# Performance work log

Hardware: AMD Instinct MI355X
Metric: run time of the kernel (lower is better)

The kernel has to match this reference:

```python
import jax, jax.numpy as jnp
import numpy as np

B, T, D = 4, 2048, 1024
H = 16
HD = D // H  # 64


def setup_inputs() -> dict:
    key = jax.random.key(0)
    ks = jax.random.split(key, 7)
    scale = 1.0 / np.sqrt(D)
    x = jax.random.normal(ks[0], (B, T, D), dtype=jnp.float32)
    # per-head projection weights, stacked over heads: [H, D, HD]
    Wq = jax.random.normal(ks[1], (H, D, HD), dtype=jnp.float32) * scale
    Wk = jax.random.normal(ks[2], (H, D, HD), dtype=jnp.float32) * scale
    Wv = jax.random.normal(ks[3], (H, D, HD), dtype=jnp.float32) * scale
    s_raw = jnp.zeros((H,), dtype=jnp.float32)  # learnable ssmax scale per head
    proj_W = jax.random.normal(ks[4], (D, D), dtype=jnp.float32) * scale
    proj_b = jax.random.normal(ks[5], (D,), dtype=jnp.float32) * 0.01
    return {"x": x, "Wq": Wq, "Wk": Wk, "Wv": Wv, "s_raw": s_raw,
            "proj_W": proj_W, "proj_b": proj_b}


def reference(x, Wq, Wk, Wv, s_raw, proj_W, proj_b):
    # per-head q/k/v: [B, H, T, HD]
    q = jnp.einsum('btd,hde->bhte', x, Wq)
    k = jnp.einsum('btd,hde->bhte', x, Wk)
    v = jnp.einsum('btd,hde->bhte', x, Wv)

    # ssmax: q scaled by softplus(s) * log(position index, 1-based)
    logn = jnp.log(jnp.arange(1, T + 1, dtype=x.dtype))  # [T]
    s = jax.nn.softplus(s_raw)  # [H]
    q = q * (s[None, :, None, None] * logn[None, None, :, None])

    scores = jnp.einsum('bhte,bhse->bhts', q, k) * (HD ** -0.5)
    causal = jnp.tril(jnp.ones((T, T), dtype=bool))
    scores = jnp.where(causal[None, None], scores, -jnp.inf)
    w = jax.nn.softmax(scores, axis=-1)

    out = jnp.einsum('bhts,bhse->bhte', w, v)          # [B, H, T, HD]
    out = out.transpose(0, 2, 1, 3).reshape(B, T, D)    # concat heads
    return out @ proj_W.T + proj_b
```

## Files before the change

kernel.cpp:

```cpp
#include <hip/hip_runtime.h>
#include <hip/hip_bf16.h>

#define Bv 4
#define Tv 2048
#define Dv 1024
#define Hv 16
#define HDv 64
#define Mv (Bv*Tv)

typedef __hip_bfloat16 bf16;
typedef short s8v __attribute__((ext_vector_type(8)));
typedef float f4v __attribute__((ext_vector_type(4)));
typedef float f16a __attribute__((ext_vector_type(16)));

__device__ __forceinline__ unsigned short f2us(float x){
    bf16 h = __float2bfloat16(x);
    return *reinterpret_cast<unsigned short*>(&h);
}
__device__ __forceinline__ unsigned int pack2(float a, float b){
    return (unsigned int)f2us(a) | ((unsigned int)f2us(b) << 16);
}
__device__ __forceinline__ void glds16(const unsigned short* g, unsigned short* lds_base){
    __builtin_amdgcn_global_load_lds(
        (const __attribute__((address_space(1))) unsigned int*)g,
        (__attribute__((address_space(3))) unsigned int*)lds_base, 16, 0, 0);
}

__global__ void cvt_kernel(const float* __restrict__ src,
                           unsigned short* __restrict__ dst, int n4) {
    int i = blockIdx.x * 256 + threadIdx.x;
    if (i < n4) {
        float4 f = *(const float4*)(src + (size_t)i * 4);
        ushort4 o;
        o.x = f2us(f.x); o.y = f2us(f.y); o.z = f2us(f.z); o.w = f2us(f.w);
        *(ushort4*)(dst + (size_t)i * 4) = o;
    }
}

__global__ __launch_bounds__(256) void wt_kernel(
    const float* __restrict__ Wq, const float* __restrict__ Wk,
    const float* __restrict__ Wv, unsigned short* __restrict__ Wt)
{
    const int dt  = blockIdx.x;
    const int h   = blockIdx.y;
    const int sel = blockIdx.z;
    const float* W = (sel == 0) ? Wq : ((sel == 1) ? Wk : Wv);
    const float* Wh = W + (size_t)h * Dv * HDv;
    __shared__ float Tf[64][65];
    const int tid = threadIdx.x;
    for (int l = 0; l < 16; ++l) {
        int idx = tid + l * 256;
        int r = idx >> 6, e = idx & 63;
        Tf[r][e] = Wh[(size_t)(dt * 64 + r) * HDv + e];
    }
    __syncthreads();
    unsigned short* out = Wt + ((size_t)sel * Hv + h) * HDv * Dv;
    for (int l = 0; l < 16; ++l) {
        int idx = tid + l * 256;
        int e = idx >> 6, d = idx & 63;
        out[(size_t)e * Dv + dt * 64 + d] = f2us(Tf[d][e]);
    }
}

__global__ __launch_bounds__(512, 2) void qkv_8ph(
    const unsigned short* __restrict__ xb, const unsigned short* __restrict__ Wc,
    const float* __restrict__ s_raw,
    unsigned short* __restrict__ q, unsigned short* __restrict__ k,
    unsigned short* __restrict__ vT)
{
    extern __shared__ unsigned short smem[];
    const int lid  = blockIdx.x;
    const int xcd  = lid & 7;
    const int slot = lid >> 3;
    const int bm   = xcd * 4 + (slot & 3);
    const int bn   = slot >> 2;
    const int tid = threadIdx.x;
    const int w = tid >> 6, lane = tid & 63;
    const int wm = w >> 2, wn = w & 3;
    const int n16 = lane & 15, quad = lane >> 4, l7 = lane & 7;

    const int row0 = bm * 256, col0 = bn * 256;

    const int sr = lane >> 3;
    const int sc = ((lane & 7) ^ (sr & 7)) * 8;

    f4v acc[8][4];
    f4v zero = {0.f, 0.f, 0.f, 0.f};
    #pragma unroll
    for (int i = 0; i < 8; ++i)
        #pragma unroll
        for (int j = 0; j < 4; ++j) acc[i][j] = zero;

    s8v Ar[8][2];
    s8v Br[4][2];

    auto stageA = [&](int b, int h, int tk){
        const unsigned short* g = xb + ((size_t)(row0 + h*128 + w*16 + sr)) * Dv + tk*64 + sc;
        unsigned short* l = smem + b*32768 + h*8192 + w*1024;
        glds16(g, l);
        glds16(g + 8*Dv, l + 512);
    };
    auto stageB = [&](int b, int h, int tk){
        const unsigned short* g = Wc + ((size_t)(col0 + h*128 + w*16 + sr)) * Dv + tk*64 + sc;
        unsigned short* l = smem + b*32768 + 16384 + h*8192 + w*1024;
        glds16(g, l);
        glds16(g + 8*Dv, l + 512);
    };
    auto readA = [&](int b, int mh){
        #pragma unroll
        for (int mi = 0; mi < 4; ++mi)
            #pragma unroll
            for (int kk = 0; kk < 2; ++kk)
                Ar[mh*4+mi][kk] = *(const s8v*)(smem + b*32768 + wm*8192
                    + ((mh*4+mi)*16 + n16) * 64 + (((kk*4 + quad) ^ l7) * 8));
    };
    auto readB = [&](int b, int nh){
        #pragma unroll
        for (int ni = 0; ni < 2; ++ni)
            #pragma unroll
            for (int kk = 0; kk < 2; ++kk)
                Br[nh*2+ni][kk] = *(const s8v*)(smem + b*32768 + 16384 + (wn>>1)*8192
                    + ((wn&1)*64 + (nh*2+ni)*16 + n16) * 64 + (((kk*4 + quad) ^ l7) * 8));
    };
    auto quadMM = [&](int mh, int nh){
        #pragma unroll
        for (int kk = 0; kk < 2; ++kk)
            #pragma unroll
            for (int mi = 0; mi < 4; ++mi)
                #pragma unroll
                for (int ni = 0; ni < 2; ++ni)
                    acc[mh*4+mi][nh*2+ni] = __builtin_amdgcn_mfma_f32_16x16x32_bf16(
                        Ar[mh*4+mi][kk], Br[nh*2+ni][kk], acc[mh*4+mi][nh*2+ni], 0, 0, 0);
    };

    stageA(0,0,0); stageA(0,1,0); stageB(0,0,0); stageB(0,1,0);
    stageA(1,0,1); stageA(1,1,1); stageB(1,0,1); stageB(1,1,1);
    asm volatile("s_waitcnt vmcnt(8)" ::: "memory");
    __builtin_amdgcn_s_barrier();

    #pragma unroll 1
    for (int it = 0; it < 8; ++it) {
        const int t2 = (2*it + 2) & 15, t3 = (2*it + 3) & 15;
        readA(0,0); readB(0,0);
        __builtin_amdgcn_s_barrier();
        __builtin_amdgcn_s_setprio(1); quadMM(0,0); __builtin_amdgcn_s_setprio(0);
        __builtin_amdgcn_s_barrier();
        readB(0,1); readA(0,1);
        __builtin_amdgcn_s_barrier();
        __builtin_amdgcn_s_setprio(1); quadMM(0,1); __builtin_amdgcn_s_setprio(0);
        asm volatile("s_waitcnt lgkmcnt(0)" ::: "memory");
        __builtin_amdgcn_s_barrier();
        stageA(0,0,t2);
        __builtin_amdgcn_s_barrier();
        __builtin_amdgcn_s_setprio(1); quadMM(1,0); __builtin_amdgcn_s_setprio(0);
        __builtin_amdgcn_s_barrier();
        stageA(0,1,t2);
        __builtin_amdgcn_s_barrier();
        __builtin_amdgcn_s_setprio(1); quadMM(1,1); __builtin_amdgcn_s_setprio(0);
        asm volatile("s_waitcnt vmcnt(4)" ::: "memory");
        __builtin_amdgcn_s_barrier();
        readA(1,0); readB(1,0); stageB(0,0,t2);
        __builtin_amdgcn_s_barrier();
        __builtin_amdgcn_s_setprio(1); quadMM(0,0); __builtin_amdgcn_s_setprio(0);
        __builtin_amdgcn_s_barrier();
        readB(1,1); readA(1,1); stageB(0,1,t2);
        __builtin_amdgcn_s_barrier();
        __builtin_amdgcn_s_setprio(1); quadMM(0,1); __builtin_amdgcn_s_setprio(0);
        asm volatile("s_waitcnt lgkmcnt(0)" ::: "memory");
        __builtin_amdgcn_s_barrier();
        stageA(1,0,t3); stageA(1,1,t3);
        __builtin_amdgcn_s_barrier();
        __builtin_amdgcn_s_setprio(1); quadMM(1,0); __builtin_amdgcn_s_setprio(0);
        __builtin_amdgcn_s_barrier();
        stageB(1,0,t3); stageB(1,1,t3);
        __builtin_amdgcn_s_barrier();
        __builtin_amdgcn_s_setprio(1); quadMM(1,1); __builtin_amdgcn_s_setprio(0);
        asm volatile("s_waitcnt vmcnt(8)" ::: "memory");
        __builtin_amdgcn_s_barrier();
    }

    const int sel = bn >> 2;
    const int h = (bn * 4 + wn) & 15;
    if (sel == 2) {
        #pragma unroll
        for (int ni = 0; ni < 4; ++ni) {
            int e = ni * 16 + n16;
            #pragma unroll
            for (int mi = 0; mi < 8; ++mi) {
                int row = row0 + wm * 128 + mi * 16 + quad * 4;
                int bb_ = row >> 11, t = row & (Tv - 1);
                ushort4 o4;
                o4.x = f2us(acc[mi][ni][0]); o4.y = f2us(acc[mi][ni][1]);
                o4.z = f2us(acc[mi][ni][2]); o4.w = f2us(acc[mi][ni][3]);
                *(ushort4*)(vT + ((size_t)(bb_ * Hv + h) * HDv + e) * Tv + t) = o4;
            }
        }
    } else {
        unsigned short* outp = (sel == 0) ? q : k;
        const float sc_h = (sel == 0) ? log1pf(expf(s_raw[h])) * 0.125f : 1.0f;
        #pragma unroll
        for (int ni = 0; ni < 4; ++ni) {
            int e = ni * 16 + n16;
            #pragma unroll
            for (int mi = 0; mi < 8; ++mi) {
                #pragma unroll
                for (int r = 0; r < 4; ++r) {
                    int row = row0 + wm * 128 + mi * 16 + quad * 4 + r;
                    int bb_ = row >> 11, t = row & (Tv - 1);
                    float rs = (sel == 0) ? sc_h * __logf((float)(t + 1)) : 1.0f;
                    outp[((size_t)(bb_ * Hv + h) * Tv + t) * HDv + e] = f2us(acc[mi][ni][r] * rs);
                }
            }
        }
    }
}

__global__ __launch_bounds__(256) void attn_mfma(
    const unsigned short* __restrict__ q, const unsigned short* __restrict__ k,
    const unsigned short* __restrict__ vT, unsigned short* __restrict__ attn)
{
    const int bh = blockIdx.y;
    const int b = bh >> 4, h = bh & 15;
    const int tid = threadIdx.x;
    const int w = tid >> 6, lane = tid & 63;
    const int l31 = lane & 31, hi = lane >> 5;

    __shared__ __align__(16) unsigned short Ks[128][72];
    __shared__ __align__(16) unsigned short VTs[64][136];

    const size_t hb = (size_t)(b * Hv + h) * Tv * HDv;
    const unsigned short* kb = k + hb;
    const unsigned short* vb = vT + hb;

    for (int phase = 0; phase < 2; ++phase) {
        const int qt = phase ? (15 - (int)blockIdx.x) : (int)blockIdx.x;
        const int qstrip = qt * 128 + w * 32;
        const int myq = qstrip + l31;

        s8v qf[4];
        #pragma unroll
        for (int ks = 0; ks < 4; ++ks)
            qf[ks] = *(const s8v*)(q + hb + (size_t)myq * HDv + ks * 16 + hi * 8);

        f16a st[4], ot0, ot1;
        #pragma unroll
        for (int i = 0; i < 16; ++i) { ot0[i] = 0.f; ot1[i] = 0.f; }
        float lrun = 0.f;

        for (int ss = 0; ss <= qt; ++ss) {
            const int s0 = ss * 128;
            __syncthreads();
            #pragma unroll
            for (int l = 0; l < 4; ++l) {
                int idx = tid + l * 256;
                int r = idx >> 3, c = (idx & 7) * 8;
                *(ulonglong2*)(&Ks[r][c]) =
                    *(const ulonglong2*)(kb + (size_t)(s0 + r) * HDv + c);
            }
            #pragma unroll
            for (int l = 0; l < 4; ++l) {
                int idx = tid + l * 256;
                int e = idx >> 4, c = (idx & 15) * 8;
                *(ulonglong2*)(&VTs[e][c]) =
                    *(const ulonglong2*)(vb + (size_t)e * Tv + s0 + c);
            }
            __syncthreads();

            #pragma unroll
            for (int mt = 0; mt < 4; ++mt)
                #pragma unroll
                for (int i = 0; i < 16; ++i) st[mt][i] = 0.f;
            #pragma unroll
            for (int ks = 0; ks < 4; ++ks) {
                #pragma unroll
                for (int mt = 0; mt < 4; ++mt) {
                    s8v a = *(const s8v*)(&Ks[32 * mt + l31][ks * 16 + hi * 8]);
                    st[mt] = __builtin_amdgcn_mfma_f32_32x32x16_bf16(a, qf[ks], st[mt], 0, 0, 0);
                }
            }
            if (s0 + 127 > qstrip) {
                #pragma unroll
                for (int mt = 0; mt < 4; ++mt)
                    #pragma unroll
                    for (int reg = 0; reg < 16; ++reg) {
                        int srow = (reg & 3) + 8 * (reg >> 2) + 4 * hi;
                        if (s0 + 32 * mt + srow > myq) st[mt][reg] = -1e30f;
                    }
            }
            float lsum = 0.f;
            #pragma unroll
            for (int mt = 0; mt < 4; ++mt)
                #pragma unroll
                for (int i = 0; i < 16; ++i) {
                    st[mt][i] = __expf(st[mt][i]);
                    lsum += st[mt][i];
                }
            lrun += lsum;

            #pragma unroll
            for (int half = 0; half < 2; ++half) {
                unsigned int pk[16];
                #pragma unroll
                for (int g = 0; g < 4; ++g) {
                    pk[2*g]       = pack2(st[2*half][4*g],     st[2*half][4*g+1]);
                    pk[2*g+1]     = pack2(st[2*half][4*g+2],   st[2*half][4*g+3]);
                    pk[8+2*g]     = pack2(st[2*half+1][4*g],   st[2*half+1][4*g+1]);
                    pk[8+2*g+1]   = pack2(st[2*half+1][4*g+2], st[2*half+1][4*g+3]);
                }
                #pragma unroll
                for (int ks4 = 0; ks4 < 4; ++ks4) {
                    const int ks = half * 4 + ks4;
                    const int base = (ks4 >> 1) * 8 + (ks4 & 1) * 4;
                    unsigned int v0 = hi ? pk[base]     : pk[base + 2];
                    unsigned int v1 = hi ? pk[base + 1] : pk[base + 3];
                    unsigned int r0 = (unsigned int)__shfl_xor((int)v0, 32);
                    unsigned int r1 = (unsigned int)__shfl_xor((int)v1, 32);
                    union { s8v v; unsigned int d[4]; } bf;
                    bf.d[0] = hi ? r0 : pk[base];
                    bf.d[1] = hi ? r1 : pk[base + 1];
                    bf.d[2] = hi ? pk[base + 2] : r0;
                    bf.d[3] = hi ? pk[base + 3] : r1;
                    s8v a0 = *(const s8v*)(&VTs[l31][ks * 16 + hi * 8]);
                    s8v a1 = *(const s8v*)(&VTs[32 + l31][ks * 16 + hi * 8]);
                    ot0 = __builtin_amdgcn_mfma_f32_32x32x16_bf16(a0, bf.v, ot0, 0, 0, 0);
                    ot1 = __builtin_amdgcn_mfma_f32_32x32x16_bf16(a1, bf.v, ot1, 0, 0, 0);
                }
            }
        }

        float ltot = lrun + __shfl_xor(lrun, 32);
        float inv = 1.0f / ltot;
        size_t obase = ((size_t)(b * Tv) + myq) * Dv + h * HDv;
        #pragma unroll
        for (int g = 0; g < 4; ++g) {
            ushort4 o4;
            o4.x = f2us(ot0[4*g]   * inv); o4.y = f2us(ot0[4*g+1] * inv);
            o4.z = f2us(ot0[4*g+2] * inv); o4.w = f2us(ot0[4*g+3] * inv);
            *(ushort4*)(attn + obase + 8 * g + 4 * hi) = o4;
            o4.x = f2us(ot1[4*g]   * inv); o4.y = f2us(ot1[4*g+1] * inv);
            o4.z = f2us(ot1[4*g+2] * inv); o4.w = f2us(ot1[4*g+3] * inv);
            *(ushort4*)(attn + obase + 32 + 8 * g + 4 * hi) = o4;
        }
    }
}

__global__ __launch_bounds__(256) void proj_big(
    const unsigned short* __restrict__ attn, const unsigned short* __restrict__ Wb,
    const float* __restrict__ bias, float* __restrict__ out)
{
    const int bm = blockIdx.x;
    const int bn = blockIdx.y;
    const int tid = threadIdx.x;
    const int w = tid >> 6, lane = tid & 63;
    const int n16 = lane & 15, quad = lane >> 4;
    const int wm = w >> 1, wn = w & 1;

    __shared__ __align__(16) unsigned short As[128 * 64];
    __shared__ __align__(16) unsigned short Bs[128 * 64];

    f4v acc[4][4];
    f4v zero = {0.f, 0.f, 0.f, 0.f};
    #pragma unroll
    for (int i = 0; i < 4; ++i)
        #pragma unroll
        for (int j = 0; j < 4; ++j) acc[i][j] = zero;

    const int row0 = bm * 128, col0 = bn * 128;
    const int lr = lane >> 3, lc = (lane & 7) * 8;

    for (int k0 = 0; k0 < Dv; k0 += 64) {
        __syncthreads();
        #pragma unroll
        for (int i = 0; i < 4; ++i) {
            int rb = w * 32 + i * 8;
            glds16(attn + (size_t)(row0 + rb + lr) * Dv + k0 + lc, &As[rb * 64]);
            glds16(Wb   + (size_t)(col0 + rb + lr) * Dv + k0 + lc, &Bs[rb * 64]);
        }
        __syncthreads();
        #pragma unroll
        for (int ks = 0; ks < 2; ++ks) {
            s8v bfr[4];
            #pragma unroll
            for (int ni = 0; ni < 4; ++ni)
                bfr[ni] = *(const s8v*)(&Bs[(wn * 64 + ni * 16 + n16) * 64 + ks * 32 + quad * 8]);
            #pragma unroll
            for (int mi = 0; mi < 4; ++mi) {
                s8v afr = *(const s8v*)(&As[(wm * 64 + mi * 16 + n16) * 64 + ks * 32 + quad * 8]);
                #pragma unroll
                for (int ni = 0; ni < 4; ++ni)
                    acc[mi][ni] = __builtin_amdgcn_mfma_f32_16x16x32_bf16(afr, bfr[ni], acc[mi][ni], 0, 0, 0);
            }
        }
    }
    #pragma unroll
    for (int ni = 0; ni < 4; ++ni) {
        int n = col0 + wn * 64 + ni * 16 + n16;
        float bn_ = bias[n];
        #pragma unroll
        for (int mi = 0; mi < 4; ++mi) {
            #pragma unroll
            for (int r = 0; r < 4; ++r) {
                int m = row0 + wm * 64 + mi * 16 + quad * 4 + r;
                out[(size_t)m * Dv + n] = acc[mi][ni][r] + bn_;
            }
        }
    }
}

extern "C" void kernel_launch(void* const* d_in, const int* in_sizes, int n_in,
                              void* d_out, int out_size, void* d_ws, size_t ws_size,
                              hipStream_t stream) {
    const float* x     = (const float*)d_in[0];
    const float* Wq    = (const float*)d_in[1];
    const float* Wk    = (const float*)d_in[2];
    const float* Wv    = (const float*)d_in[3];
    const float* s_raw = (const float*)d_in[4];
    const float* projW = (const float*)d_in[5];
    const float* projb = (const float*)d_in[6];
    float* out = (float*)d_out;

    const size_t nx  = (size_t)Mv * Dv;
    const size_t nqk = (size_t)Bv * Hv * Tv * HDv;
    unsigned short* x_bf = (unsigned short*)d_ws;
    unsigned short* qb   = x_bf + nx;
    unsigned short* kb   = qb + nqk;
    unsigned short* vTb  = kb + nqk;
    unsigned short* Wt   = vTb + nqk;
    unsigned short* Wpb  = Wt + (size_t)3 * Hv * HDv * Dv;
    unsigned short* attn = x_bf;

    static int cfg = 0;
    if (!cfg) {
        (void)hipFuncSetAttribute((const void*)qkv_8ph,
                                  hipFuncAttributeMaxDynamicSharedMemorySize, 131072);
        cfg = 1;
    }

    cvt_kernel<<<(int)(nx / 4 / 256), 256, 0, stream>>>(x, x_bf, (int)(nx / 4));
    cvt_kernel<<<(int)((size_t)Dv * Dv / 4 / 256), 256, 0, stream>>>(projW, Wpb, Dv * Dv / 4);
    wt_kernel<<<dim3(16, 16, 3), 256, 0, stream>>>(Wq, Wk, Wv, Wt);
    qkv_8ph<<<dim3(384), 512, 131072, stream>>>(x_bf, Wt, s_raw, qb, kb, vTb);
    attn_mfma<<<dim3(8, Bv * Hv), 256, 0, stream>>>(qb, kb, vTb, attn);
    proj_big<<<dim3(Mv / 128, Dv / 128), 256, 0, stream>>>(attn, Wpb, projb, out);
}
```

Baseline: 268.3 us.

## Prefetch next K/V tile into registers and remap attention blocks by XCD

The attention kernel now loads the next 128-row K and V^T tile from global memory into registers while the current tile is being computed. At the next iteration those registers are stored to LDS, so global-load latency overlaps the MFMA work. The grid is also flattened to 1D and the block index is decoded so that all blocks sharing one (batch, head) land on the same XCD, improving L2 reuse of K/V. In exchange the kernel holds eight more 16-byte registers per thread, which may lower occupancy.

```diff
diff --git a/kernel.cpp b/kernel.cpp
--- a/kernel.cpp
+++ b/kernel.cpp
@@ -197,7 +197,7 @@
         }
     } else {
         unsigned short* outp = (sel == 0) ? q : k;
-        const float sc_h = (sel == 0) ? log1pf(expf(s_raw[h])) * 0.125f : 1.0f;
+        float sc_h = (sel == 0) ? log1pf(expf(s_raw[h])) * 0.125f : 1.0f;
         #pragma unroll
         for (int ni = 0; ni < 4; ++ni) {
             int e = ni * 16 + n16;
@@ -219,7 +219,11 @@
     const unsigned short* __restrict__ q, const unsigned short* __restrict__ k,
     const unsigned short* __restrict__ vT, unsigned short* __restrict__ attn)
 {
-    const int bh = blockIdx.y;
+    const int lid = blockIdx.x;
+    const int xcd = lid & 7;
+    const int rr  = lid >> 3;
+    const int qx  = rr >> 3;
+    const int bh  = ((rr & 7) << 3) | xcd;
     const int b = bh >> 4, h = bh & 15;
     const int tid = threadIdx.x;
     const int w = tid >> 6, lane = tid & 63;
@@ -232,8 +236,11 @@
     const unsigned short* kb = k + hb;
     const unsigned short* vb = vT + hb;
 
+    const int kr0 = tid >> 3,  kc0 = (tid & 7) * 8;
+    const int ve0 = tid >> 4,  vc0 = (tid & 15) * 8;
+
     for (int phase = 0; phase < 2; ++phase) {
-        const int qt = phase ? (15 - (int)blockIdx.x) : (int)blockIdx.x;
+        const int qt = phase ? (15 - qx) : qx;
         const int qstrip = qt * 128 + w * 32;
         const int myq = qstrip + l31;
 
@@ -246,25 +253,32 @@
         #pragma unroll
         for (int i = 0; i < 16; ++i) { ot0[i] = 0.f; ot1[i] = 0.f; }
         float lrun = 0.f;
+
+        ulonglong2 kreg[4], vreg[4];
+        #pragma unroll
+        for (int l = 0; l < 4; ++l) {
+            kreg[l] = *(const ulonglong2*)(kb + (size_t)(kr0 + l * 32) * HDv + kc0);
+            vreg[l] = *(const ulonglong2*)(vb + (size_t)(ve0 + l * 16) * Tv + vc0);
+        }
 
         for (int ss = 0; ss <= qt; ++ss) {
             const int s0 = ss * 128;
             __syncthreads();
             #pragma unroll
-            for (int l = 0; l < 4; ++l) {
-                int idx = tid + l * 256;
-                int r = idx >> 3, c = (idx & 7) * 8;
-                *(ulonglong2*)(&Ks[r][c]) =
-                    *(const ulonglong2*)(kb + (size_t)(s0 + r) * HDv + c);
-            }
-            #pragma unroll
-            for (int l = 0; l < 4; ++l) {
-                int idx = tid + l * 256;
-                int e = idx >> 4, c = (idx & 15) * 8;
-                *(ulonglong2*)(&VTs[e][c]) =
-                    *(const ulonglong2*)(vb + (size_t)e * Tv + s0 + c);
-            }
+            for (int l = 0; l < 4; ++l)
+                *(ulonglong2*)(&Ks[kr0 + l * 32][kc0]) = kreg[l];
+            #pragma unroll
+            for (int l = 0; l < 4; ++l)
+                *(ulonglong2*)(&VTs[ve0 + l * 16][vc0]) = vreg[l];
             __syncthreads();
+            if (ss < qt) {
+                const int s1 = s0 + 128;
+                #pragma unroll
+                for (int l = 0; l < 4; ++l) {
+                    kreg[l] = *(const ulonglong2*)(kb + (size_t)(s1 + kr0 + l * 32) * HDv + kc0);
+                    vreg[l] = *(const ulonglong2*)(vb + (size_t)(ve0 + l * 16) * Tv + s1 + vc0);
+                }
+            }
 
             #pragma unroll
             for (int mt = 0; mt < 4; ++mt)
@@ -440,6 +454,6 @@
     cvt_kernel<<<(int)((size_t)Dv * Dv / 4 / 256), 256, 0, stream>>>(projW, Wpb, Dv * Dv / 4);
     wt_kernel<<<dim3(16, 16, 3), 256, 0, stream>>>(Wq, Wk, Wv, Wt);
     qkv_8ph<<<dim3(384), 512, 131072, stream>>>(x_bf, Wt, s_raw, qb, kb, vTb);
-    attn_mfma<<<dim3(8, Bv * Hv), 256, 0, stream>>>(qb, kb, vTb, attn);
+    attn_mfma<<<dim3(512), 256, 0, stream>>>(qb, kb, vTb, attn);
     proj_big<<<dim3(Mv / 128, Dv / 128), 256, 0, stream>>>(attn, Wpb, projb, out);
 }
```

New measurement: 321.4 us. +19.8%, slower.
